# Performance work log

Hardware: AMD Instinct MI355X
Metric: run time of the kernel (lower is better)

Reference implementation:

```python
import jax, jax.numpy as jnp
import numpy as np

D_MODEL = 768
N_HEADS = 12
D_FF = 3072
EPS = 1e-5


def _layernorm(x, g, b):
    mu = jnp.mean(x, axis=-1, keepdims=True)
    var = jnp.mean(jnp.square(x - mu), axis=-1, keepdims=True)
    return (x - mu) * jax.lax.rsqrt(var + EPS) * g + b


def setup_inputs() -> dict:
    key = jax.random.key(0)
    ks = jax.random.split(key, 16)
    d, f = D_MODEL, D_FF
    s = 1.0 / np.sqrt(d)
    inp = {
        "x": jax.random.normal(ks[0], (1, 4096, d), dtype=jnp.float32),
        "Wq": jax.random.normal(ks[1], (d, d), dtype=jnp.float32) * s,
        "bq": jnp.zeros((d,), jnp.float32),
        "Wk": jax.random.normal(ks[2], (d, d), dtype=jnp.float32) * s,
        "bk": jnp.zeros((d,), jnp.float32),
        "Wv": jax.random.normal(ks[3], (d, d), dtype=jnp.float32) * s,
        "bv": jnp.zeros((d,), jnp.float32),
        "Wo": jax.random.normal(ks[4], (d, d), dtype=jnp.float32) * s,
        "bo": jnp.zeros((d,), jnp.float32),
        "ln1_g": jnp.ones((d,), jnp.float32),
        "ln1_b": jnp.zeros((d,), jnp.float32),
        "ln2_g": jnp.ones((d,), jnp.float32),
        "ln2_b": jnp.zeros((d,), jnp.float32),
        "W1": jax.random.normal(ks[5], (d, f), dtype=jnp.float32) * s,
        "b1": jnp.zeros((f,), jnp.float32),
        "W2": jax.random.normal(ks[6], (f, d), dtype=jnp.float32) * (1.0 / np.sqrt(f)),
        "b2": jnp.zeros((d,), jnp.float32),
    }
    return inp


def reference(x, Wq, bq, Wk, bk, Wv, bv, Wo, bo, ln1_g, ln1_b, ln2_g, ln2_b, W1, b1, W2, b2):
    b, s, d = x.shape
    h = N_HEADS
    dk = d // h

    # --- attention sublayer (pre-norm residual) ---
    xn = _layernorm(x, ln1_g, ln1_b)

    def proj(W, bias):
        y = xn @ W + bias                      # [b, s, d]
        return y.reshape(b, s, h, dk).transpose(0, 2, 1, 3)  # [b, h, s, dk]

    q, k, v = proj(Wq, bq), proj(Wk, bk), proj(Wv, bv)
    scores = jnp.einsum("bhqd,bhkd->bhqk", q, k) / np.sqrt(dk)
    attn = jax.nn.softmax(scores, axis=-1)
    ctx = jnp.einsum("bhqk,bhkd->bhqd", attn, v)
    ctx = ctx.transpose(0, 2, 1, 3).reshape(b, s, d)
    x = x + (ctx @ Wo + bo)

    # --- FFN sublayer (pre-norm residual) ---
    xn2 = _layernorm(x, ln2_g, ln2_b)
    ff = jax.nn.gelu(xn2 @ W1 + b1, approximate=False) @ W2 + b2
    return x + ff
```

## Files before the change

### kernel.cpp

```cpp
#include <hip/hip_runtime.h>
#include <hip/hip_bf16.h>

typedef __attribute__((ext_vector_type(8))) __bf16 bf16x8;
typedef __attribute__((ext_vector_type(4))) __bf16 bf16x4;
typedef __attribute__((ext_vector_type(4))) float f32x4;
typedef __attribute__((ext_vector_type(4))) unsigned short u16x4;
typedef unsigned short ushort_t;

__device__ __forceinline__ ushort_t f2bf(float f) {
    union { float f; unsigned u; } v; v.f = f;
    unsigned r = v.u + 0x7fffu + ((v.u >> 16) & 1u);
    return (ushort_t)(r >> 16);
}

__device__ __forceinline__ void gload16(const ushort_t* g, ushort_t* l) {
    __builtin_amdgcn_global_load_lds(
        (const __attribute__((address_space(1))) unsigned int*)g,
        (__attribute__((address_space(3))) unsigned int*)l,
        16, 0, 0);
}

__global__ __launch_bounds__(256) void ln_kernel(const float* __restrict__ x,
                                                 const float* __restrict__ g,
                                                 const float* __restrict__ b,
                                                 ushort_t* __restrict__ out) {
    const int row = blockIdx.x;
    const float* xr = x + (size_t)row * 768;
    const int t = threadIdx.x;
    float v0 = xr[t], v1 = xr[t + 256], v2 = xr[t + 512];
    float s  = v0 + v1 + v2;
    float s2 = v0 * v0 + v1 * v1 + v2 * v2;
#pragma unroll
    for (int off = 32; off; off >>= 1) {
        s  += __shfl_down(s, off);
        s2 += __shfl_down(s2, off);
    }
    __shared__ float red[8];
    const int wid = t >> 6, lane = t & 63;
    if (lane == 0) { red[wid] = s; red[4 + wid] = s2; }
    __syncthreads();
    __shared__ float stats[2];
    if (t == 0) {
        float S = red[0] + red[1] + red[2] + red[3];
        float S2 = red[4] + red[5] + red[6] + red[7];
        float mu = S * (1.0f / 768.0f);
        float var = S2 * (1.0f / 768.0f) - mu * mu;
        stats[0] = mu;
        stats[1] = rsqrtf(var + 1e-5f);
    }
    __syncthreads();
    const float mu = stats[0], rs = stats[1];
    ushort_t* orow = out + (size_t)row * 768;
    orow[t]       = f2bf((v0 - mu) * rs * g[t]       + b[t]);
    orow[t + 256] = f2bf((v1 - mu) * rs * g[t + 256] + b[t + 256]);
    orow[t + 512] = f2bf((v2 - mu) * rs * g[t + 512] + b[t + 512]);
}

__global__ __launch_bounds__(256) void prep_weights(
    const float* __restrict__ Wq, const float* __restrict__ Wk,
    const float* __restrict__ Wv, const float* __restrict__ Wo,
    const float* __restrict__ W1, const float* __restrict__ W2,
    const float* __restrict__ bq, const float* __restrict__ bk,
    const float* __restrict__ bv,
    ushort_t* __restrict__ WqkvT, ushort_t* __restrict__ WoT,
    ushort_t* __restrict__ W1T, ushort_t* __restrict__ W2T,
    float* __restrict__ bqkv) {
    const int bid = blockIdx.x;
    const int t = threadIdx.x;
    if (bid >= 6912) {
        const int i = bid - 6912;
        const float* s = (i == 0) ? bq : (i == 1) ? bk : bv;
#pragma unroll
        for (int j = t; j < 768; j += 256) bqkv[i * 768 + j] = s[j];
        return;
    }
    const float* src; ushort_t* dst; int R, C, ti;
    if (bid < 576)       { src = Wq; dst = WqkvT;               R = 768;  C = 768;  ti = bid; }
    else if (bid < 1152) { src = Wk; dst = WqkvT + 768 * 768;   R = 768;  C = 768;  ti = bid - 576; }
    else if (bid < 1728) { src = Wv; dst = WqkvT + 2 * 768 * 768; R = 768; C = 768; ti = bid - 1152; }
    else if (bid < 2304) { src = Wo; dst = WoT;                 R = 768;  C = 768;  ti = bid - 1728; }
    else if (bid < 4608) { src = W1; dst = W1T;                 R = 768;  C = 3072; ti = bid - 2304; }
    else                 { src = W2; dst = W2T;                 R = 3072; C = 768;  ti = bid - 4608; }
    const int tpr = C >> 5;
    const int c0 = (ti % tpr) * 32, r0 = (ti / tpr) * 32;
    __shared__ float tile[32][33];
    {
        const int c = t & 31, r = t >> 5;
#pragma unroll
        for (int i = 0; i < 4; i++)
            tile[r + i * 8][c] = src[(size_t)(r0 + r + i * 8) * C + c0 + c];
    }
    __syncthreads();
    {
        const int oc = t >> 3, q = t & 7;
        u16x4 o;
#pragma unroll
        for (int k = 0; k < 4; k++) o[k] = f2bf(tile[q * 4 + k][oc]);
        *(u16x4*)&dst[(size_t)(c0 + oc) * R + r0 + q * 4] = o;
    }
}

template <int BN, int GELU, int RES, int OUTF, int OUTB, int OUTV>
__global__ __launch_bounds__(256, 3)
void gemm_bt(const ushort_t* __restrict__ A, const ushort_t* __restrict__ Bt,
             const float* __restrict__ bias, const float* __restrict__ res,
             float* __restrict__ outF, ushort_t* __restrict__ outB, int ldo,
             ushort_t* __restrict__ outV,
             int M, int N, int K) {
    constexpr int TR  = 128 + BN;
    constexpr int LL  = TR / 64;
    constexpr int WCF = BN / 32;
    __shared__ __align__(16) ushort_t Ls[2][TR * 32];

    const int nbx = gridDim.x;
    const int nwg = nbx * gridDim.y;
    int fb = blockIdx.y * nbx + blockIdx.x;
    fb = (fb & 7) * (nwg >> 3) + (fb >> 3);
    const int m0 = (fb / nbx) * 128, n0 = (fb % nbx) * BN;

    const int t = threadIdx.x;
    const int wid = t >> 6, lane = t & 63;
    const int wr = wid >> 1, wc = wid & 1;
    const int row16 = lane & 15, kg = lane >> 4;
    const int kb = kg * 8;

    const int srow = lane >> 2, scol = (lane & 3) * 8;
    const ushort_t* gsrc[LL];
    int lofs[LL];
#pragma unroll
    for (int i = 0; i < LL; i++) {
        const int r0 = wid * (TR / 4) + 16 * i;
        gsrc[i] = (r0 < 128 ? A + (size_t)(m0 + r0 + srow) * K
                            : Bt + (size_t)(n0 + r0 - 128 + srow) * K) + scol;
        lofs[i] = r0 * 32;
    }

#define STAGE(buf, kofs) do {                                        \
        _Pragma("unroll")                                            \
        for (int i = 0; i < LL; i++)                                 \
            gload16(gsrc[i] + (kofs), &Ls[buf][lofs[i]]);            \
    } while (0)

    f32x4 acc[4][WCF] = {};
    const int NS = K >> 5;
    STAGE(0, 0);
    STAGE(1, 32);
    int cur = 0;

    for (int s = 0; s < NS; ++s) {
        if (s + 1 == NS) asm volatile("s_waitcnt vmcnt(0)" ::: "memory");
        else             asm volatile("s_waitcnt vmcnt(%0)" :: "i"(LL) : "memory");
        __builtin_amdgcn_s_barrier();

        bf16x8 a[4], b[WCF];
#pragma unroll
        for (int i = 0; i < 4; i++)
            a[i] = *(const bf16x8*)&Ls[cur][(wr * 64 + i * 16 + row16) * 32 + kb];
#pragma unroll
        for (int j = 0; j < WCF; j++)
            b[j] = *(const bf16x8*)&Ls[cur][(128 + wc * (BN / 2) + j * 16 + row16) * 32 + kb];
        asm volatile("s_waitcnt lgkmcnt(0)" ::: "memory");
        __builtin_amdgcn_s_barrier();
        if (s + 2 < NS) STAGE(cur, (s + 2) * 32);

        __builtin_amdgcn_s_setprio(1);
#pragma unroll
        for (int i = 0; i < 4; i++)
#pragma unroll
            for (int j = 0; j < WCF; j++)
                acc[i][j] = __builtin_amdgcn_mfma_f32_16x16x32_bf16(a[i], b[j], acc[i][j], 0, 0, 0);
        __builtin_amdgcn_s_setprio(0);
        cur ^= 1;
    }
#undef STAGE

#pragma unroll
    for (int i = 0; i < 4; i++)
#pragma unroll
        for (int j = 0; j < WCF; j++) {
            const int col = n0 + wc * (BN / 2) + j * 16 + row16;
            const float bv = bias[col];
            const int rb = m0 + wr * 64 + i * 16 + kg * 4;
            if (OUTV && col >= 1536) {
                bf16x4 pk;
#pragma unroll
                for (int r = 0; r < 4; r++) pk[r] = (__bf16)(acc[i][j][r] + bv);
                *(bf16x4*)&outV[(size_t)(col - 1536) * 4096 + rb] = pk;
            } else {
#pragma unroll
                for (int r = 0; r < 4; r++) {
                    const int row = rb + r;
                    float v = acc[i][j][r] + bv;
                    if (GELU) v = 0.5f * v * (1.0f + erff(v * 0.70710678118654752f));
                    if (RES) v += res[(size_t)row * N + col];
                    if (OUTF) outF[(size_t)row * N + col] = v;
                    if (OUTB) outB[(size_t)row * ldo + col] = f2bf(v);
                }
            }
        }
}

__device__ __forceinline__ int swz(int row, int col) {
    return row * 64 + (col ^ ((row & 7) << 3));
}

__global__ __launch_bounds__(256, 3)
void attn_kernel(const ushort_t* __restrict__ qk,
                 const ushort_t* __restrict__ Vt,
                 ushort_t* __restrict__ ctx) {
    int fb = blockIdx.y * 64 + blockIdx.x;
    fb = (fb & 7) * 96 + (fb >> 3);
    const int q0 = (fb & 63) * 64;
    const int h  = fb >> 6;

    const int t  = threadIdx.x;
    const int w = t >> 6, lane = t & 63;
    const int row16 = lane & 15, kg = lane >> 4;
    const int kb = kg * 8;

    __shared__ ushort_t Qs[64 * 64];
    __shared__ ushort_t Ks[2][64 * 64];
    __shared__ ushort_t Vs[2][64 * 64];
    ushort_t* Ps = Qs;

    const int sr = t >> 2, sc = (t & 3) * 8;

    {
        const size_t qb = (size_t)(q0 + sr) * 1536 + h * 64 + sc;
        *(uint4*)&Qs[swz(sr, sc)]      = *(const uint4*)&qk[qb];
        *(uint4*)&Qs[swz(sr, sc + 32)] = *(const uint4*)&qk[qb + 32];
        const size_t kbase = (size_t)sr * 1536 + 768 + h * 64 + sc;
        *(uint4*)&Ks[0][swz(sr, sc)]      = *(const uint4*)&qk[kbase];
        *(uint4*)&Ks[0][swz(sr, sc + 32)] = *(const uint4*)&qk[kbase + 32];
        const size_t vbase = (size_t)(h * 64 + sr) * 4096 + sc;
        *(uint4*)&Vs[0][swz(sr, sc)]      = *(const uint4*)&Vt[vbase];
        *(uint4*)&Vs[0][swz(sr, sc + 32)] = *(const uint4*)&Vt[vbase + 32];
    }
    const bf16x8 qa0 = *(const bf16x8*)&Qs[swz(w * 16 + row16, kb)];
    const bf16x8 qa1 = *(const bf16x8*)&Qs[swz(w * 16 + row16, 32 + kb)];
    __syncthreads();

    f32x4 o_acc[4] = {};
    float m_r = -1e30f, l_r = 0.0f;
    int cur = 0;
    const float SC = 0.18033688011112042f;

    for (int it = 0; it < 64; ++it) {
        uint4 k0r, k1r, v0r, v1r;
        const bool pf = (it < 63);
        if (pf) {
            const int kv1 = (it + 1) * 64;
            const size_t kbase = (size_t)(kv1 + sr) * 1536 + 768 + h * 64 + sc;
            k0r = *(const uint4*)&qk[kbase];
            k1r = *(const uint4*)&qk[kbase + 32];
            const size_t vbase = (size_t)(h * 64 + sr) * 4096 + kv1 + sc;
            v0r = *(const uint4*)&Vt[vbase];
            v1r = *(const uint4*)&Vt[vbase + 32];
        }

        const ushort_t* Kc = Ks[cur];
        const ushort_t* Vc = Vs[cur];

        f32x4 s_acc[4];
        __builtin_amdgcn_s_setprio(1);
#pragma unroll
        for (int f = 0; f < 4; f++) {
            bf16x8 ka0 = *(const bf16x8*)&Kc[swz(f * 16 + row16, kb)];
            bf16x8 ka1 = *(const bf16x8*)&Kc[swz(f * 16 + row16, 32 + kb)];
            f32x4 z = {};
            z = __builtin_amdgcn_mfma_f32_16x16x32_bf16(ka0, qa0, z, 0, 0, 0);
            s_acc[f] = __builtin_amdgcn_mfma_f32_16x16x32_bf16(ka1, qa1, z, 0, 0, 0);
        }
        __builtin_amdgcn_s_setprio(0);

        float tmx = s_acc[0][0];
#pragma unroll
        for (int f = 0; f < 4; f++)
#pragma unroll
            for (int r = 0; r < 4; r++) tmx = fmaxf(tmx, s_acc[f][r]);

        if (!__all(tmx * SC <= m_r + 8.0f)) {
            float tmax = fmaxf(tmx, __shfl_xor(tmx, 16));
            tmax = fmaxf(tmax, __shfl_xor(tmax, 32));
            const float m_new = fmaxf(m_r, tmax * SC);
            const float alpha = __builtin_amdgcn_exp2f(m_r - m_new);
            l_r *= alpha;
            float alpha_pv[4];
#pragma unroll
            for (int r = 0; r < 4; r++) alpha_pv[r] = __shfl(alpha, kg * 4 + r);
#pragma unroll
            for (int f = 0; f < 4; f++)
#pragma unroll
                for (int r = 0; r < 4; r++) o_acc[f][r] *= alpha_pv[r];
            m_r = m_new;
        }

        float p[4][4];
        float rsum = 0.0f;
#pragma unroll
        for (int f = 0; f < 4; f++)
#pragma unroll
            for (int r = 0; r < 4; r++) {
                p[f][r] = __builtin_amdgcn_exp2f(fmaf(s_acc[f][r], SC, -m_r));
                rsum += p[f][r];
            }
        rsum += __shfl_xor(rsum, 16);
        rsum += __shfl_xor(rsum, 32);
        l_r += rsum;

#pragma unroll
        for (int f = 0; f < 4; f++) {
            bf16x4 pk;
            pk[0] = (__bf16)p[f][0];
            pk[1] = (__bf16)p[f][1];
            pk[2] = (__bf16)p[f][2];
            pk[3] = (__bf16)p[f][3];
            *(bf16x4*)&Ps[swz(w * 16 + row16, f * 16 + kg * 4)] = pk;
        }

        const bf16x8 pa0 = *(const bf16x8*)&Ps[swz(w * 16 + row16, kb)];
        const bf16x8 pa1 = *(const bf16x8*)&Ps[swz(w * 16 + row16, 32 + kb)];
        __builtin_amdgcn_s_setprio(1);
#pragma unroll
        for (int f = 0; f < 4; f++) {
            bf16x8 vb0 = *(const bf16x8*)&Vc[swz(f * 16 + row16, kb)];
            bf16x8 vb1 = *(const bf16x8*)&Vc[swz(f * 16 + row16, 32 + kb)];
            o_acc[f] = __builtin_amdgcn_mfma_f32_16x16x32_bf16(pa0, vb0, o_acc[f], 0, 0, 0);
            o_acc[f] = __builtin_amdgcn_mfma_f32_16x16x32_bf16(pa1, vb1, o_acc[f], 0, 0, 0);
        }
        __builtin_amdgcn_s_setprio(0);

        if (pf) {
            *(uint4*)&Ks[cur ^ 1][swz(sr, sc)]      = k0r;
            *(uint4*)&Ks[cur ^ 1][swz(sr, sc + 32)] = k1r;
            *(uint4*)&Vs[cur ^ 1][swz(sr, sc)]      = v0r;
            *(uint4*)&Vs[cur ^ 1][swz(sr, sc + 32)] = v1r;
        }
        __syncthreads();
        cur ^= 1;
    }

    float l_pv[4];
#pragma unroll
    for (int r = 0; r < 4; r++) l_pv[r] = __shfl(l_r, kg * 4 + r);
#pragma unroll
    for (int f = 0; f < 4; f++)
#pragma unroll
        for (int r = 0; r < 4; r++) {
            const int qrow = q0 + w * 16 + kg * 4 + r;
            ctx[(size_t)qrow * 768 + h * 64 + f * 16 + row16] = f2bf(o_acc[f][r] / l_pv[r]);
        }
}

extern "C" void kernel_launch(void* const* d_in, const int* in_sizes, int n_in,
                              void* d_out, int out_size, void* d_ws, size_t ws_size,
                              hipStream_t stream) {
    const float* x     = (const float*)d_in[0];
    const float* Wq    = (const float*)d_in[1];
    const float* bq    = (const float*)d_in[2];
    const float* Wk    = (const float*)d_in[3];
    const float* bk    = (const float*)d_in[4];
    const float* Wv    = (const float*)d_in[5];
    const float* bv    = (const float*)d_in[6];
    const float* Wo    = (const float*)d_in[7];
    const float* bo    = (const float*)d_in[8];
    const float* ln1_g = (const float*)d_in[9];
    const float* ln1_b = (const float*)d_in[10];
    const float* ln2_g = (const float*)d_in[11];
    const float* ln2_b = (const float*)d_in[12];
    const float* W1    = (const float*)d_in[13];
    const float* b1    = (const float*)d_in[14];
    const float* W2    = (const float*)d_in[15];
    const float* b2    = (const float*)d_in[16];

    char* ws = (char*)d_ws;
    ushort_t* WqkvT = (ushort_t*)ws; ws += (size_t)2304 * 768 * 2;
    ushort_t* WoT   = (ushort_t*)ws; ws += (size_t)768 * 768 * 2;
    ushort_t* W1T   = (ushort_t*)ws; ws += (size_t)3072 * 768 * 2;
    ushort_t* W2T   = (ushort_t*)ws; ws += (size_t)768 * 3072 * 2;
    float*    bqkv  = (float*)ws;    ws += (size_t)2304 * 4;
    ushort_t* xn    = (ushort_t*)ws; ws += (size_t)4096 * 768 * 2;
    ushort_t* qk    = (ushort_t*)ws; ws += (size_t)4096 * 1536 * 2;
    ushort_t* Vtb   = (ushort_t*)ws; ws += (size_t)768 * 4096 * 2;
    ushort_t* ctxb  = (ushort_t*)ws; ws += (size_t)4096 * 768 * 2;
    float*    x1    = (float*)ws;    ws += (size_t)4096 * 768 * 4;
    ushort_t* H     = qk;

    prep_weights<<<6915, 256, 0, stream>>>(Wq, Wk, Wv, Wo, W1, W2, bq, bk, bv,
                                           WqkvT, WoT, W1T, W2T, bqkv);

    ln_kernel<<<4096, 256, 0, stream>>>(x, ln1_g, ln1_b, xn);
    gemm_bt<128, 0, 0, 0, 1, 1><<<dim3(18, 32), 256, 0, stream>>>(
        xn, WqkvT, bqkv, nullptr, nullptr, qk, 1536, Vtb, 4096, 2304, 768);

    attn_kernel<<<dim3(64, 12), 256, 0, stream>>>(qk, Vtb, ctxb);

    gemm_bt<64, 0, 1, 1, 0, 0><<<dim3(12, 32), 256, 0, stream>>>(
        ctxb, WoT, bo, x, x1, nullptr, 0, nullptr, 4096, 768, 768);

    ln_kernel<<<4096, 256, 0, stream>>>(x1, ln2_g, ln2_b, xn);
    gemm_bt<128, 1, 0, 0, 1, 0><<<dim3(24, 32), 256, 0, stream>>>(
        xn, W1T, b1, nullptr, nullptr, H, 3072, nullptr, 4096, 3072, 768);
    gemm_bt<64, 0, 1, 1, 0, 0><<<dim3(12, 32), 256, 0, stream>>>(
        H, W2T, b2, x1, (float*)d_out, nullptr, 0, nullptr, 4096, 768, 3072);

    (void)in_sizes; (void)n_in; (void)out_size; (void)ws_size;
}
```

Measured before the change: 225.0 us.

## Fuse LN1 into weight prep, async LDS loads and MFMA row-sum in attention

Merges the first layernorm into the weight-prep launch so one kernel launch is removed. The attention K/V prefetch now uses global_load_lds straight into shared memory with a swizzled column pattern, replacing register staging and separate LDS stores. The softmax row sum is computed by an extra MFMA against a vector of ones instead of scalar exp sums and shuffles. This removes VALU and shuffle work but adds two MFMAs per tile and accumulates the denominator from bf16-rounded probabilities.

```diff
diff --git a/kernel.cpp b/kernel.cpp
--- a/kernel.cpp
+++ b/kernel.cpp
@@ -20,13 +20,10 @@
         16, 0, 0);
 }
 
-__global__ __launch_bounds__(256) void ln_kernel(const float* __restrict__ x,
-                                                 const float* __restrict__ g,
-                                                 const float* __restrict__ b,
-                                                 ushort_t* __restrict__ out) {
-    const int row = blockIdx.x;
-    const float* xr = x + (size_t)row * 768;
-    const int t = threadIdx.x;
+__device__ __forceinline__ void ln_row(const float* __restrict__ xr,
+                                       const float* __restrict__ g,
+                                       const float* __restrict__ b,
+                                       ushort_t* __restrict__ orow, int t) {
     float v0 = xr[t], v1 = xr[t + 256], v2 = xr[t + 512];
     float s  = v0 + v1 + v2;
     float s2 = v0 * v0 + v1 * v1 + v2 * v2;
@@ -50,23 +47,37 @@
     }
     __syncthreads();
     const float mu = stats[0], rs = stats[1];
-    ushort_t* orow = out + (size_t)row * 768;
     orow[t]       = f2bf((v0 - mu) * rs * g[t]       + b[t]);
     orow[t + 256] = f2bf((v1 - mu) * rs * g[t + 256] + b[t + 256]);
     orow[t + 512] = f2bf((v2 - mu) * rs * g[t + 512] + b[t + 512]);
 }
 
-__global__ __launch_bounds__(256) void prep_weights(
+__global__ __launch_bounds__(256) void ln_kernel(const float* __restrict__ x,
+                                                 const float* __restrict__ g,
+                                                 const float* __restrict__ b,
+                                                 ushort_t* __restrict__ out) {
+    const int row = blockIdx.x;
+    ln_row(x + (size_t)row * 768, g, b, out + (size_t)row * 768, threadIdx.x);
+}
+
+__global__ __launch_bounds__(256) void prep_ln(
     const float* __restrict__ Wq, const float* __restrict__ Wk,
     const float* __restrict__ Wv, const float* __restrict__ Wo,
     const float* __restrict__ W1, const float* __restrict__ W2,
     const float* __restrict__ bq, const float* __restrict__ bk,
     const float* __restrict__ bv,
+    const float* __restrict__ x, const float* __restrict__ ln1_g,
+    const float* __restrict__ ln1_b,
     ushort_t* __restrict__ WqkvT, ushort_t* __restrict__ WoT,
     ushort_t* __restrict__ W1T, ushort_t* __restrict__ W2T,
-    float* __restrict__ bqkv) {
+    float* __restrict__ bqkv, ushort_t* __restrict__ xn) {
     const int bid = blockIdx.x;
     const int t = threadIdx.x;
+    if (bid >= 6915) {
+        const int row = bid - 6915;
+        ln_row(x + (size_t)row * 768, ln1_g, ln1_b, xn + (size_t)row * 768, t);
+        return;
+    }
     if (bid >= 6912) {
         const int i = bid - 6912;
         const float* s = (i == 0) ? bq : (i == 1) ? bk : bv;
@@ -218,9 +229,9 @@
     const int row16 = lane & 15, kg = lane >> 4;
     const int kb = kg * 8;
 
-    __shared__ ushort_t Qs[64 * 64];
-    __shared__ ushort_t Ks[2][64 * 64];
-    __shared__ ushort_t Vs[2][64 * 64];
+    __shared__ __align__(16) ushort_t Qs[64 * 64];
+    __shared__ __align__(16) ushort_t Ks[2][64 * 64];
+    __shared__ __align__(16) ushort_t Vs[2][64 * 64];
     ushort_t* Ps = Qs;
 
     const int sr = t >> 2, sc = (t & 3) * 8;
@@ -240,22 +251,30 @@
     const bf16x8 qa1 = *(const bf16x8*)&Qs[swz(w * 16 + row16, 32 + kb)];
     __syncthreads();
 
+    const int rr = lane >> 3;
+    const int gcol = ((lane & 7) ^ rr) * 8;
+    const ushort_t* gK = qk + 768 + h * 64 + gcol + (size_t)(w * 16 + rr) * 1536;
+    const ushort_t* gV = Vt + (size_t)(h * 64 + w * 16 + rr) * 4096 + gcol;
+
+    bf16x8 vones;
+#pragma unroll
+    for (int i = 0; i < 8; i++) vones[i] = (__bf16)1.0f;
+
     f32x4 o_acc[4] = {};
-    float m_r = -1e30f, l_r = 0.0f;
+    f32x4 o_l = {};
+    float m_r = -1e30f;
     int cur = 0;
     const float SC = 0.18033688011112042f;
 
     for (int it = 0; it < 64; ++it) {
-        uint4 k0r, k1r, v0r, v1r;
-        const bool pf = (it < 63);
-        if (pf) {
+        if (it != 63) {
             const int kv1 = (it + 1) * 64;
-            const size_t kbase = (size_t)(kv1 + sr) * 1536 + 768 + h * 64 + sc;
-            k0r = *(const uint4*)&qk[kbase];
-            k1r = *(const uint4*)&qk[kbase + 32];
-            const size_t vbase = (size_t)(h * 64 + sr) * 4096 + kv1 + sc;
-            v0r = *(const uint4*)&Vt[vbase];
-            v1r = *(const uint4*)&Vt[vbase + 32];
+            ushort_t* kd = &Ks[cur ^ 1][w * 1024];
+            ushort_t* vd = &Vs[cur ^ 1][w * 1024];
+            gload16(gK + (size_t)kv1 * 1536,       kd);
+            gload16(gK + (size_t)(kv1 + 8) * 1536, kd + 512);
+            gload16(gV + kv1,                      vd);
+            gload16(gV + kv1 + 8 * 4096,           vd + 512);
         }
 
         const ushort_t* Kc = Ks[cur];
@@ -284,7 +303,6 @@
             tmax = fmaxf(tmax, __shfl_xor(tmax, 32));
             const float m_new = fmaxf(m_r, tmax * SC);
             const float alpha = __builtin_amdgcn_exp2f(m_r - m_new);
-            l_r *= alpha;
             float alpha_pv[4];
 #pragma unroll
             for (int r = 0; r < 4; r++) alpha_pv[r] = __shfl(alpha, kg * 4 + r);
@@ -292,29 +310,17 @@
             for (int f = 0; f < 4; f++)
 #pragma unroll
                 for (int r = 0; r < 4; r++) o_acc[f][r] *= alpha_pv[r];
+#pragma unroll
+            for (int r = 0; r < 4; r++) o_l[r] *= alpha_pv[r];
             m_r = m_new;
         }
-
-        float p[4][4];
-        float rsum = 0.0f;
-#pragma unroll
-        for (int f = 0; f < 4; f++)
-#pragma unroll
-            for (int r = 0; r < 4; r++) {
-                p[f][r] = __builtin_amdgcn_exp2f(fmaf(s_acc[f][r], SC, -m_r));
-                rsum += p[f][r];
-            }
-        rsum += __shfl_xor(rsum, 16);
-        rsum += __shfl_xor(rsum, 32);
-        l_r += rsum;
 
 #pragma unroll
         for (int f = 0; f < 4; f++) {
             bf16x4 pk;
-            pk[0] = (__bf16)p[f][0];
-            pk[1] = (__bf16)p[f][1];
-            pk[2] = (__bf16)p[f][2];
-            pk[3] = (__bf16)p[f][3];
+#pragma unroll
+            for (int r = 0; r < 4; r++)
+                pk[r] = (__bf16)__builtin_amdgcn_exp2f(fmaf(s_acc[f][r], SC, -m_r));
             *(bf16x4*)&Ps[swz(w * 16 + row16, f * 16 + kg * 4)] = pk;
         }
 
@@ -328,27 +334,20 @@
             o_acc[f] = __builtin_amdgcn_mfma_f32_16x16x32_bf16(pa0, vb0, o_acc[f], 0, 0, 0);
             o_acc[f] = __builtin_amdgcn_mfma_f32_16x16x32_bf16(pa1, vb1, o_acc[f], 0, 0, 0);
         }
+        o_l = __builtin_amdgcn_mfma_f32_16x16x32_bf16(pa0, vones, o_l, 0, 0, 0);
+        o_l = __builtin_amdgcn_mfma_f32_16x16x32_bf16(pa1, vones, o_l, 0, 0, 0);
         __builtin_amdgcn_s_setprio(0);
 
-        if (pf) {
-            *(uint4*)&Ks[cur ^ 1][swz(sr, sc)]      = k0r;
-            *(uint4*)&Ks[cur ^ 1][swz(sr, sc + 32)] = k1r;
-            *(uint4*)&Vs[cur ^ 1][swz(sr, sc)]      = v0r;
-            *(uint4*)&Vs[cur ^ 1][swz(sr, sc + 32)] = v1r;
-        }
         __syncthreads();
         cur ^= 1;
     }
 
-    float l_pv[4];
-#pragma unroll
-    for (int r = 0; r < 4; r++) l_pv[r] = __shfl(l_r, kg * 4 + r);
 #pragma unroll
     for (int f = 0; f < 4; f++)
 #pragma unroll
         for (int r = 0; r < 4; r++) {
             const int qrow = q0 + w * 16 + kg * 4 + r;
-            ctx[(size_t)qrow * 768 + h * 64 + f * 16 + row16] = f2bf(o_acc[f][r] / l_pv[r]);
+            ctx[(size_t)qrow * 768 + h * 64 + f * 16 + row16] = f2bf(o_acc[f][r] / o_l[r]);
         }
 }
 
@@ -386,10 +385,10 @@
     float*    x1    = (float*)ws;    ws += (size_t)4096 * 768 * 4;
     ushort_t* H     = qk;
 
-    prep_weights<<<6915, 256, 0, stream>>>(Wq, Wk, Wv, Wo, W1, W2, bq, bk, bv,
-                                           WqkvT, WoT, W1T, W2T, bqkv);
-
-    ln_kernel<<<4096, 256, 0, stream>>>(x, ln1_g, ln1_b, xn);
+    prep_ln<<<6915 + 4096, 256, 0, stream>>>(Wq, Wk, Wv, Wo, W1, W2, bq, bk, bv,
+                                             x, ln1_g, ln1_b,
+                                             WqkvT, WoT, W1T, W2T, bqkv, xn);
+
     gemm_bt<128, 0, 0, 0, 1, 1><<<dim3(18, 32), 256, 0, stream>>>(
         xn, WqkvT, bqkv, nullptr, nullptr, qk, 1536, Vtb, 4096, 2304, 768);
 
```

Result: faster. 213.7 us (-5.0%).
